# Optimization experiments

Measured on AMD Instinct MI355X. Metric: run time of the kernel, lower is better.

## Reference

```python
import jax, jax.numpy as jnp
import numpy as np

MOMENTUM = 0.5  # update_method='momentum'
EPS = 1e-12


def _l2norm(x):
    return x / jnp.sqrt(jnp.sum(x * x, axis=-1, keepdims=True) + EPS)


def setup_inputs() -> dict:
    key = jax.random.key(0)
    k1, k2, k3, k4, k5 = jax.random.split(key, 5)
    N, D, C, B = 200000, 256, 1000, 256
    inputs = _l2norm(jax.random.normal(k1, (B, D), dtype=jnp.float32))
    features = _l2norm(jax.random.normal(k2, (N, D), dtype=jnp.float32))
    cluster_mean = jax.random.normal(k3, (C, D), dtype=jnp.float32)
    labels = jax.random.randint(k4, (N,), 0, C)
    indexes = jax.random.randint(k5, (B,), 0, N)
    targets = labels[indexes]  # cluster id of each mini-batch sample
    return {
        "inputs": inputs,
        "features": features,
        "cluster_mean": cluster_mean,
        "indexes": indexes,
        "labels": labels,
        "targets": targets,
    }


def reference(inputs, features, cluster_mean, indexes, labels, targets):
    # HM.forward: logits against cluster centroids
    outputs = inputs @ cluster_mean.T  # [B, C]

    # HM.backward side effects (memory-bank maintenance), vectorized:
    # 1) momentum scatter update of the per-instance memory bank + L2 renorm
    new_rows = MOMENTUM * features[indexes] + (1.0 - MOMENTUM) * inputs
    new_rows = _l2norm(new_rows)
    feats = features.at[indexes].set(new_rows)

    # 2) naive cluster-mean recompute (get_mean_conv mean part) for touched clusters
    C = cluster_mean.shape[0]
    sums = jax.ops.segment_sum(feats, labels, num_segments=C)            # [C, D]
    cnts = jax.ops.segment_sum(jnp.ones((feats.shape[0],), feats.dtype), labels, num_segments=C)
    means = sums / jnp.maximum(cnts, 1.0)[:, None]
    touched = jnp.zeros((C,), dtype=bool).at[targets].set(True)
    new_cluster_mean = jnp.where(touched[:, None], means, cluster_mean)

    return outputs, feats, new_cluster_mean
```

## Files before the change

### kernel.cpp

```cpp
#include <hip/hip_runtime.h>

typedef float f32x4 __attribute__((ext_vector_type(4)));

#define B 256
#define D 256
#define N 200000
#define C 1000

#define K1_BLOCKS   2048
#define LOGITS_LO   0
#define NEWROWS_LO  256
#define TOUCH_BLK   512
#define HIST_LO     513
#define HIST_BLOCKS 64
#define COPY_LO     577
#define COPY_BLOCKS (K1_BLOCKS - COPY_LO)

#define WS_NEWROWS_OFF  0
#define WS_HIST_OFF     262144
#define WS_TOUCHED_OFF  266144
#define WS_NW_OFF       270144
#define WS_OFFS_OFF     270148
#define WS_FILLPOS_OFF  274148
#define WS_WROW_OFF     278148
#define WS_WLAB_OFF     279172
#define WS_WB_OFF       280196
#define WS_ROWLIST_OFF  281220
#define ZERO_WORDS      (2 * C + 1)

__global__ __launch_bounds__(256) void k0_zero(int* __restrict__ z) {
    int i = blockIdx.x * 256 + threadIdx.x;
    if (i < ZERO_WORDS) z[i] = 0;
}

__global__ __launch_bounds__(256) void k1_kernel(
    const float* __restrict__ inputs, const float* __restrict__ features,
    const float* __restrict__ cluster_mean, const int* __restrict__ indexes,
    const int* __restrict__ labels, const int* __restrict__ targets,
    float* __restrict__ out_logits, float* __restrict__ out_feats,
    float* __restrict__ new_rows, int* __restrict__ hist, int* __restrict__ touched)
{
    const int blk = blockIdx.x;
    const int t = threadIdx.x;

    if (blk >= COPY_LO) {
        const f32x4* src = (const f32x4*)features;
        f32x4*       dst = (f32x4*)out_feats;
        const int total4 = N * (D / 4);
        const int stride = COPY_BLOCKS * 256;
        int i = (blk - COPY_LO) * 256 + t;
        for (; i + 3 * stride < total4; i += 4 * stride) {
            f32x4 v0 = src[i];
            f32x4 v1 = src[i + stride];
            f32x4 v2 = src[i + 2 * stride];
            f32x4 v3 = src[i + 3 * stride];
            __builtin_nontemporal_store(v0, dst + i);
            __builtin_nontemporal_store(v1, dst + i + stride);
            __builtin_nontemporal_store(v2, dst + i + 2 * stride);
            __builtin_nontemporal_store(v3, dst + i + 3 * stride);
        }
        for (; i < total4; i += stride)
            __builtin_nontemporal_store(src[i], dst + i);
    } else if (blk < NEWROWS_LO) {
        __shared__ float sbuf[D];
        int b = blk - LOGITS_LO;
        sbuf[t] = inputs[b * D + t];
        __syncthreads();
        const f32x4* cmv = (const f32x4*)cluster_mean;
        for (int c = t; c < C; c += 256) {
            const f32x4* cm = cmv + (size_t)c * 64;
            float a0 = 0.f, a1 = 0.f, a2 = 0.f, a3 = 0.f;
            #pragma unroll 8
            for (int d4 = 0; d4 < 64; ++d4) {
                f32x4 v = cm[d4];
                const float* si = sbuf + d4 * 4;
                a0 += v.x * si[0];
                a1 += v.y * si[1];
                a2 += v.z * si[2];
                a3 += v.w * si[3];
            }
            out_logits[(size_t)b * C + c] = (a0 + a1) + (a2 + a3);
        }
    } else if (blk < TOUCH_BLK) {
        __shared__ float wpart[4];
        __shared__ float stot;
        int b = blk - NEWROWS_LO;
        int r = indexes[b];
        float x = 0.5f * features[(size_t)r * D + t] + 0.5f * inputs[b * D + t];
        float s = x * x;
        #pragma unroll
        for (int off = 32; off > 0; off >>= 1) s += __shfl_down(s, off);
        if ((t & 63) == 0) wpart[t >> 6] = s;
        __syncthreads();
        if (t == 0) stot = (wpart[0] + wpart[1]) + (wpart[2] + wpart[3]);
        __syncthreads();
        new_rows[b * D + t] = x / sqrtf(stot + 1e-12f);
    } else if (blk == TOUCH_BLK) {
        if (t < B) touched[targets[t]] = 1;
    } else {
        __shared__ int lh[C];
        for (int i = t; i < C; i += 256) lh[i] = 0;
        __syncthreads();
        const int stride = HIST_BLOCKS * 256;
        for (int i = (blk - HIST_LO) * 256 + t; i < N; i += stride)
            atomicAdd(&lh[labels[i]], 1);
        __syncthreads();
        for (int i = t; i < C; i += 256) {
            int v = lh[i];
            if (v) atomicAdd(&hist[i], v);
        }
    }
}

__global__ __launch_bounds__(256) void k2_kernel(
    const int* __restrict__ indexes, const int* __restrict__ labels,
    const float* __restrict__ new_rows, float* __restrict__ out_feats,
    const int* __restrict__ hist, int* __restrict__ offs, int* __restrict__ fillpos,
    int* __restrict__ nw, int* __restrict__ w_row, int* __restrict__ w_lab,
    int* __restrict__ w_b)
{
    const int blk = blockIdx.x;
    const int t = threadIdx.x;

    if (blk < 256) {
        __shared__ int sidx[B];
        __shared__ int lose;
        sidx[t] = indexes[t];
        if (t == 0) lose = 0;
        __syncthreads();
        int b = blk;
        int my = sidx[b];
        if (t > b && sidx[t] == my) lose = 1;
        __syncthreads();
        if (!lose) {
            __builtin_nontemporal_store(new_rows[b * D + t], &out_feats[(size_t)my * D + t]);
            if (t == 0) {
                int p = atomicAdd(nw, 1);
                w_row[p] = my;
                w_lab[p] = labels[my];
                w_b[p] = b;
            }
        }
    } else {
        __shared__ int swt[4];
        int base = t * 4;
        int h0 = (base + 0 < C) ? hist[base + 0] : 0;
        int h1 = (base + 1 < C) ? hist[base + 1] : 0;
        int h2 = (base + 2 < C) ? hist[base + 2] : 0;
        int h3 = (base + 3 < C) ? hist[base + 3] : 0;
        int tot = h0 + h1 + h2 + h3;
        int lane = t & 63;
        int scan = tot;
        #pragma unroll
        for (int off = 1; off < 64; off <<= 1) {
            int v = __shfl_up(scan, off);
            if (lane >= off) scan += v;
        }
        if (lane == 63) swt[t >> 6] = scan;
        __syncthreads();
        int wbase = 0;
        for (int i = 0; i < (t >> 6); ++i) wbase += swt[i];
        int excl = wbase + scan - tot;
        if (base + 0 < C) { offs[base + 0] = excl;                fillpos[base + 0] = excl; }
        if (base + 1 < C) { offs[base + 1] = excl + h0;           fillpos[base + 1] = excl + h0; }
        if (base + 2 < C) { offs[base + 2] = excl + h0 + h1;      fillpos[base + 2] = excl + h0 + h1; }
        if (base + 3 < C) { offs[base + 3] = excl + h0 + h1 + h2; fillpos[base + 3] = excl + h0 + h1 + h2; }
    }
}

__global__ __launch_bounds__(256) void fill_kernel(
    const int* __restrict__ labels, const int* __restrict__ touched,
    int* __restrict__ fillpos, int* __restrict__ rowlist)
{
    int i = blockIdx.x * 256 + threadIdx.x;
    if (i >= N) return;
    int lab = labels[i];
    if (touched[lab]) {
        int p = atomicAdd(&fillpos[lab], 1);
        rowlist[p] = i;
    }
}

__global__ __launch_bounds__(1024) void cm_kernel(
    const float* __restrict__ cluster_mean, const float* __restrict__ features,
    const float* __restrict__ new_rows, const int* __restrict__ touched,
    const int* __restrict__ hist, const int* __restrict__ offs,
    const int* __restrict__ rowlist, const int* __restrict__ nw,
    const int* __restrict__ w_row, const int* __restrict__ w_lab,
    const int* __restrict__ w_b, float* __restrict__ out_cm)
{
    const int c = blockIdx.x;
    const int d = threadIdx.x & 255;
    const int k = threadIdx.x >> 8;
    if (!touched[c]) {
        if (k == 0) out_cm[(size_t)c * D + d] = cluster_mean[(size_t)c * D + d];
        return;
    }
    __shared__ float red[3][256];
    const int cnt = hist[c];
    const int off = offs[c];
    float acc = 0.0f;
    #pragma unroll 4
    for (int j = k; j < cnt; j += 4)
        acc += features[(size_t)rowlist[off + j] * D + d];
    const int nwv = *nw;
    for (int j = k; j < nwv; j += 4) {
        if (w_lab[j] == c)
            acc += new_rows[w_b[j] * D + d] - features[(size_t)w_row[j] * D + d];
    }
    if (k > 0) red[k - 1][d] = acc;
    __syncthreads();
    if (k == 0) {
        float tot = acc + red[0][d] + red[1][d] + red[2][d];
        out_cm[(size_t)c * D + d] = tot / fmaxf((float)cnt, 1.0f);
    }
}

extern "C" void kernel_launch(void* const* d_in, const int* in_sizes, int n_in,
                              void* d_out, int out_size, void* d_ws, size_t ws_size,
                              hipStream_t stream) {
    const float* inputs       = (const float*)d_in[0];
    const float* features     = (const float*)d_in[1];
    const float* cluster_mean = (const float*)d_in[2];
    const int*   indexes      = (const int*)d_in[3];
    const int*   labels       = (const int*)d_in[4];
    const int*   targets      = (const int*)d_in[5];

    float* out_logits = (float*)d_out;
    float* out_feats  = out_logits + (size_t)B * C;
    float* out_cm     = out_feats + (size_t)N * D;

    char* ws = (char*)d_ws;
    float* new_rows = (float*)(ws + WS_NEWROWS_OFF);
    int*   hist     = (int*)(ws + WS_HIST_OFF);
    int*   touched  = (int*)(ws + WS_TOUCHED_OFF);
    int*   nw       = (int*)(ws + WS_NW_OFF);
    int*   offs     = (int*)(ws + WS_OFFS_OFF);
    int*   fillpos  = (int*)(ws + WS_FILLPOS_OFF);
    int*   w_row    = (int*)(ws + WS_WROW_OFF);
    int*   w_lab    = (int*)(ws + WS_WLAB_OFF);
    int*   w_b      = (int*)(ws + WS_WB_OFF);
    int*   rowlist  = (int*)(ws + WS_ROWLIST_OFF);

    k0_zero<<<(ZERO_WORDS + 255) / 256, 256, 0, stream>>>((int*)(ws + WS_HIST_OFF));
    k1_kernel<<<K1_BLOCKS, 256, 0, stream>>>(inputs, features, cluster_mean,
                                             indexes, labels, targets,
                                             out_logits, out_feats, new_rows,
                                             hist, touched);
    k2_kernel<<<257, 256, 0, stream>>>(indexes, labels, new_rows, out_feats,
                                       hist, offs, fillpos, nw, w_row, w_lab, w_b);
    fill_kernel<<<(N + 255) / 256, 256, 0, stream>>>(labels, touched, fillpos, rowlist);
    cm_kernel<<<C, 1024, 0, stream>>>(cluster_mean, features, new_rows, touched,
                                      hist, offs, rowlist, nw, w_row, w_lab, w_b,
                                      out_cm);
}
```

Before: 124.7 us.

## Drop zeroing kernel via per-block histograms and move winner detection into k1

The separate zero-init launch is removed. Each histogram block now writes its own partial histogram to workspace with plain stores instead of global atomics, and block 0 of k2 sums the 64 partials before the scan. Duplicate-index winner detection and touched-flag clearing move into one block of k1, so k2 only scatters the winning new rows. Copy blocks are also moved to the front of the grid. This trades one kernel launch and the global atomics for a serial 64-way reduction in k2 and a single block doing O(B²) duplicate checks.

```diff
diff --git a/kernel.cpp b/kernel.cpp
--- a/kernel.cpp
+++ b/kernel.cpp
@@ -8,47 +8,43 @@
 #define C 1000
 
 #define K1_BLOCKS   2048
-#define LOGITS_LO   0
-#define NEWROWS_LO  256
-#define TOUCH_BLK   512
-#define HIST_LO     513
+#define COPY_BLOCKS 1471
+#define LOGITS_LO   1471
+#define NEWROWS_LO  1727
+#define WIN_BLK     1983
+#define HIST_LO     1984
 #define HIST_BLOCKS 64
-#define COPY_LO     577
-#define COPY_BLOCKS (K1_BLOCKS - COPY_LO)
 
 #define WS_NEWROWS_OFF  0
-#define WS_HIST_OFF     262144
-#define WS_TOUCHED_OFF  266144
-#define WS_NW_OFF       270144
-#define WS_OFFS_OFF     270148
-#define WS_FILLPOS_OFF  274148
+#define WS_NW_OFF       262144
+#define WS_OFFS_OFF     262148
+#define WS_FILLPOS_OFF  266148
+#define WS_CNTS_OFF     270148
+#define WS_TOUCHED_OFF  274148
 #define WS_WROW_OFF     278148
 #define WS_WLAB_OFF     279172
 #define WS_WB_OFF       280196
-#define WS_ROWLIST_OFF  281220
-#define ZERO_WORDS      (2 * C + 1)
-
-__global__ __launch_bounds__(256) void k0_zero(int* __restrict__ z) {
-    int i = blockIdx.x * 256 + threadIdx.x;
-    if (i < ZERO_WORDS) z[i] = 0;
-}
+#define WS_HB_OFF       281220
+#define WS_ROWLIST_OFF  537220
 
 __global__ __launch_bounds__(256) void k1_kernel(
     const float* __restrict__ inputs, const float* __restrict__ features,
     const float* __restrict__ cluster_mean, const int* __restrict__ indexes,
     const int* __restrict__ labels, const int* __restrict__ targets,
     float* __restrict__ out_logits, float* __restrict__ out_feats,
-    float* __restrict__ new_rows, int* __restrict__ hist, int* __restrict__ touched)
+    float* __restrict__ new_rows, int* __restrict__ hb, int* __restrict__ touched,
+    int* __restrict__ nw, int* __restrict__ w_row, int* __restrict__ w_lab,
+    int* __restrict__ w_b)
 {
     const int blk = blockIdx.x;
     const int t = threadIdx.x;
 
-    if (blk >= COPY_LO) {
+    if (blk < COPY_BLOCKS) {
         const f32x4* src = (const f32x4*)features;
         f32x4*       dst = (f32x4*)out_feats;
         const int total4 = N * (D / 4);
         const int stride = COPY_BLOCKS * 256;
-        int i = (blk - COPY_LO) * 256 + t;
+        int i = blk * 256 + t;
         for (; i + 3 * stride < total4; i += 4 * stride) {
             f32x4 v0 = src[i];
             f32x4 v1 = src[i + stride];
@@ -81,7 +77,7 @@
             }
             out_logits[(size_t)b * C + c] = (a0 + a1) + (a2 + a3);
         }
-    } else if (blk < TOUCH_BLK) {
+    } else if (blk < WIN_BLK) {
         __shared__ float wpart[4];
         __shared__ float stot;
         int b = blk - NEWROWS_LO;
@@ -95,59 +91,59 @@
         if (t == 0) stot = (wpart[0] + wpart[1]) + (wpart[2] + wpart[3]);
         __syncthreads();
         new_rows[b * D + t] = x / sqrtf(stot + 1e-12f);
-    } else if (blk == TOUCH_BLK) {
-        if (t < B) touched[targets[t]] = 1;
+    } else if (blk == WIN_BLK) {
+        __shared__ int sidx[B];
+        __shared__ int cnt;
+        for (int i = t; i < C; i += 256) touched[i] = 0;
+        sidx[t] = indexes[t];
+        if (t == 0) cnt = 0;
+        __syncthreads();
+        touched[targets[t]] = 1;
+        bool win = true;
+        for (int j = t + 1; j < B; ++j)
+            if (sidx[j] == sidx[t]) { win = false; break; }
+        if (win) {
+            int p = atomicAdd(&cnt, 1);
+            int r = sidx[t];
+            w_row[p] = r;
+            w_lab[p] = labels[r];
+            w_b[p] = t;
+        }
+        __syncthreads();
+        if (t == 0) *nw = cnt;
     } else {
         __shared__ int lh[C];
         for (int i = t; i < C; i += 256) lh[i] = 0;
         __syncthreads();
+        const int hb_i = blk - HIST_LO;
         const int stride = HIST_BLOCKS * 256;
-        for (int i = (blk - HIST_LO) * 256 + t; i < N; i += stride)
+        for (int i = hb_i * 256 + t; i < N; i += stride)
             atomicAdd(&lh[labels[i]], 1);
         __syncthreads();
-        for (int i = t; i < C; i += 256) {
-            int v = lh[i];
-            if (v) atomicAdd(&hist[i], v);
-        }
+        for (int i = t; i < C; i += 256) hb[hb_i * C + i] = lh[i];
     }
 }
 
 __global__ __launch_bounds__(256) void k2_kernel(
-    const int* __restrict__ indexes, const int* __restrict__ labels,
     const float* __restrict__ new_rows, float* __restrict__ out_feats,
-    const int* __restrict__ hist, int* __restrict__ offs, int* __restrict__ fillpos,
-    int* __restrict__ nw, int* __restrict__ w_row, int* __restrict__ w_lab,
-    int* __restrict__ w_b)
+    const int* __restrict__ hb, int* __restrict__ offs, int* __restrict__ fillpos,
+    int* __restrict__ cnts, const int* __restrict__ nw,
+    const int* __restrict__ w_row, const int* __restrict__ w_b)
 {
     const int blk = blockIdx.x;
     const int t = threadIdx.x;
 
-    if (blk < 256) {
-        __shared__ int sidx[B];
-        __shared__ int lose;
-        sidx[t] = indexes[t];
-        if (t == 0) lose = 0;
-        __syncthreads();
-        int b = blk;
-        int my = sidx[b];
-        if (t > b && sidx[t] == my) lose = 1;
-        __syncthreads();
-        if (!lose) {
-            __builtin_nontemporal_store(new_rows[b * D + t], &out_feats[(size_t)my * D + t]);
-            if (t == 0) {
-                int p = atomicAdd(nw, 1);
-                w_row[p] = my;
-                w_lab[p] = labels[my];
-                w_b[p] = b;
-            }
-        }
-    } else {
+    if (blk == 0) {
         __shared__ int swt[4];
         int base = t * 4;
-        int h0 = (base + 0 < C) ? hist[base + 0] : 0;
-        int h1 = (base + 1 < C) ? hist[base + 1] : 0;
-        int h2 = (base + 2 < C) ? hist[base + 2] : 0;
-        int h3 = (base + 3 < C) ? hist[base + 3] : 0;
+        int h0 = 0, h1 = 0, h2 = 0, h3 = 0;
+        for (int i = 0; i < HIST_BLOCKS; ++i) {
+            const int* row = hb + i * C;
+            if (base + 0 < C) h0 += row[base + 0];
+            if (base + 1 < C) h1 += row[base + 1];
+            if (base + 2 < C) h2 += row[base + 2];
+            if (base + 3 < C) h3 += row[base + 3];
+        }
         int tot = h0 + h1 + h2 + h3;
         int lane = t & 63;
         int scan = tot;
@@ -161,10 +157,14 @@
         int wbase = 0;
         for (int i = 0; i < (t >> 6); ++i) wbase += swt[i];
         int excl = wbase + scan - tot;
-        if (base + 0 < C) { offs[base + 0] = excl;                fillpos[base + 0] = excl; }
-        if (base + 1 < C) { offs[base + 1] = excl + h0;           fillpos[base + 1] = excl + h0; }
-        if (base + 2 < C) { offs[base + 2] = excl + h0 + h1;      fillpos[base + 2] = excl + h0 + h1; }
-        if (base + 3 < C) { offs[base + 3] = excl + h0 + h1 + h2; fillpos[base + 3] = excl + h0 + h1 + h2; }
+        if (base + 0 < C) { offs[base + 0] = excl;                fillpos[base + 0] = excl;                cnts[base + 0] = h0; }
+        if (base + 1 < C) { offs[base + 1] = excl + h0;           fillpos[base + 1] = excl + h0;           cnts[base + 1] = h1; }
+        if (base + 2 < C) { offs[base + 2] = excl + h0 + h1;      fillpos[base + 2] = excl + h0 + h1;      cnts[base + 2] = h2; }
+        if (base + 3 < C) { offs[base + 3] = excl + h0 + h1 + h2; fillpos[base + 3] = excl + h0 + h1 + h2; cnts[base + 3] = h3; }
+    } else {
+        int q = blk - 1;
+        if (q < *nw)
+            out_feats[(size_t)w_row[q] * D + t] = new_rows[w_b[q] * D + t];
     }
 }
 
@@ -184,7 +184,7 @@
 __global__ __launch_bounds__(1024) void cm_kernel(
     const float* __restrict__ cluster_mean, const float* __restrict__ features,
     const float* __restrict__ new_rows, const int* __restrict__ touched,
-    const int* __restrict__ hist, const int* __restrict__ offs,
+    const int* __restrict__ cnts, const int* __restrict__ offs,
     const int* __restrict__ rowlist, const int* __restrict__ nw,
     const int* __restrict__ w_row, const int* __restrict__ w_lab,
     const int* __restrict__ w_b, float* __restrict__ out_cm)
@@ -197,7 +197,7 @@
         return;
     }
     __shared__ float red[3][256];
-    const int cnt = hist[c];
+    const int cnt = cnts[c];
     const int off = offs[c];
     float acc = 0.0f;
     #pragma unroll 4
@@ -232,25 +232,25 @@
 
     char* ws = (char*)d_ws;
     float* new_rows = (float*)(ws + WS_NEWROWS_OFF);
-    int*   hist     = (int*)(ws + WS_HIST_OFF);
-    int*   touched  = (int*)(ws + WS_TOUCHED_OFF);
     int*   nw       = (int*)(ws + WS_NW_OFF);
     int*   offs     = (int*)(ws + WS_OFFS_OFF);
     int*   fillpos  = (int*)(ws + WS_FILLPOS_OFF);
+    int*   cnts     = (int*)(ws + WS_CNTS_OFF);
+    int*   touched  = (int*)(ws + WS_TOUCHED_OFF);
     int*   w_row    = (int*)(ws + WS_WROW_OFF);
     int*   w_lab    = (int*)(ws + WS_WLAB_OFF);
     int*   w_b      = (int*)(ws + WS_WB_OFF);
+    int*   hb       = (int*)(ws + WS_HB_OFF);
     int*   rowlist  = (int*)(ws + WS_ROWLIST_OFF);
 
-    k0_zero<<<(ZERO_WORDS + 255) / 256, 256, 0, stream>>>((int*)(ws + WS_HIST_OFF));
     k1_kernel<<<K1_BLOCKS, 256, 0, stream>>>(inputs, features, cluster_mean,
                                              indexes, labels, targets,
                                              out_logits, out_feats, new_rows,
-                                             hist, touched);
-    k2_kernel<<<257, 256, 0, stream>>>(indexes, labels, new_rows, out_feats,
-                                       hist, offs, fillpos, nw, w_row, w_lab, w_b);
+                                             hb, touched, nw, w_row, w_lab, w_b);
+    k2_kernel<<<257, 256, 0, stream>>>(new_rows, out_feats, hb, offs, fillpos,
+                                       cnts, nw, w_row, w_b);
     fill_kernel<<<(N + 255) / 256, 256, 0, stream>>>(labels, touched, fillpos, rowlist);
     cm_kernel<<<C, 1024, 0, stream>>>(cluster_mean, features, new_rows, touched,
-                                      hist, offs, rowlist, nw, w_row, w_lab, w_b,
+                                      cnts, offs, rowlist, nw, w_row, w_lab, w_b,
                                       out_cm);
 }
```

Measured after the change: 166.1 us. +33.2%, slower.
